# Kernel optimization log

Measured on AMD Instinct MI355X. Metric: run time of the kernel, lower is better.

Reference implementation:

```python
import jax, jax.numpy as jnp
import numpy as np

B, S, HID = 2, 2048, 2048
H, KVH, D = 16, 4, 128
GROUPS = H // KVH
THETA = 10000.0
SCALE = 1.0 / np.sqrt(D).astype(np.float32)
NEG = -1e9


def setup_inputs() -> dict:
    key = jax.random.key(0)
    ks = jax.random.split(key, 6)
    x = jax.random.normal(ks[0], (B, S, HID), dtype=jnp.float32)
    # causal additive mask, broadcast over heads
    causal = jnp.triu(jnp.full((S, S), NEG, dtype=jnp.float32), k=1)
    attn_mask = jnp.broadcast_to(causal, (B, 1, S, S))
    pos_ids = jnp.broadcast_to(jnp.arange(S, dtype=jnp.int32), (B, S))
    sd = 0.02
    Wq = jax.random.normal(ks[1], (H * D, HID), dtype=jnp.float32) * sd
    Wk = jax.random.normal(ks[2], (KVH * D, HID), dtype=jnp.float32) * sd
    Wv = jax.random.normal(ks[3], (KVH * D, HID), dtype=jnp.float32) * sd
    Wo = jax.random.normal(ks[4], (HID, H * D), dtype=jnp.float32) * sd
    return {"x": x, "attn_mask": attn_mask, "pos_ids": pos_ids,
            "Wq": Wq, "Wk": Wk, "Wv": Wv, "Wo": Wo}


def _rope_cos_sin(pos_ids):
    # pos_ids: [B, S] -> cos/sin: [B, 1, S, D]
    inv_freq = 1.0 / (THETA ** (jnp.arange(0, D, 2, dtype=jnp.float32) / D))
    freqs = pos_ids.astype(jnp.float32)[:, :, None] * inv_freq  # [B, S, D/2]
    emb = jnp.concatenate([freqs, freqs], axis=-1)              # [B, S, D]
    return jnp.cos(emb)[:, None], jnp.sin(emb)[:, None]


def _rotate_half(t):
    t1, t2 = jnp.split(t, 2, axis=-1)
    return jnp.concatenate([-t2, t1], axis=-1)


def reference(x, attn_mask, pos_ids, Wq, Wk, Wv, Wo):
    b, s, _ = x.shape
    q = jnp.einsum('bsh,oh->bso', x, Wq).reshape(b, s, H, D).transpose(0, 2, 1, 3)
    k = jnp.einsum('bsh,oh->bso', x, Wk).reshape(b, s, KVH, D).transpose(0, 2, 1, 3)
    v = jnp.einsum('bsh,oh->bso', x, Wv).reshape(b, s, KVH, D).transpose(0, 2, 1, 3)
    cos, sin = _rope_cos_sin(pos_ids)
    q = q * cos + _rotate_half(q) * sin
    k = k * cos + _rotate_half(k) * sin
    # GQA: repeat kv heads
    k = jnp.repeat(k, GROUPS, axis=1)  # [b, H, s, D]
    v = jnp.repeat(v, GROUPS, axis=1)
    scores = jnp.einsum('bhqd,bhkd->bhqk', q, k) * SCALE + attn_mask
    weights = jax.nn.softmax(scores, axis=-1)  # dropout p=0 (eval)
    out = jnp.einsum('bhqk,bhkd->bhqd', weights, v)
    out = out.transpose(0, 2, 1, 3).reshape(b, s, H * D)
    return jnp.einsum('bso,ho->bsh', out, Wo)
```

## Files before the change

### kernel.cpp

```cpp
#include <hip/hip_runtime.h>
#include <hip/hip_bf16.h>
#include <stdint.h>

#define B_   2
#define S_   2048
#define HID_ 2048
#define H_   16
#define KVH_ 4
#define D_   128
#define SCALE_ 0.08838834764831845f
#define QSC_ (SCALE_ * 1.4426950408889634f)

typedef __attribute__((ext_vector_type(8))) short bf16x8;
typedef __attribute__((ext_vector_type(4))) float f32x4;
typedef __attribute__((ext_vector_type(4))) short short4v;

__device__ __forceinline__ void async_copy16(void* lds, const void* g) {
  __builtin_amdgcn_global_load_lds((__attribute__((address_space(1))) void*)(uintptr_t)g,
                                   (__attribute__((address_space(3))) void*)lds, 16, 0, 0);
}

__device__ __forceinline__ short bf16bits(float f) {
  __hip_bfloat16 t = __float2bfloat16(f);
  return __builtin_bit_cast(short, t);
}
__device__ __forceinline__ float bf16tof(short s) {
  return __bfloat162float(__builtin_bit_cast(__hip_bfloat16, s));
}

__global__ __launch_bounds__(256) void f2b_all(const float4* __restrict__ x,
                                               const float4* __restrict__ wq,
                                               const float4* __restrict__ wk,
                                               const float4* __restrict__ wv,
                                               const float4* __restrict__ wo,
                                               short4v* __restrict__ xb,
                                               short4v* __restrict__ wqb,
                                               short4v* __restrict__ wkb,
                                               short4v* __restrict__ wvb,
                                               short4v* __restrict__ wob) {
  int i = blockIdx.x * blockDim.x + threadIdx.x;
  const float4* src; short4v* dst; int off;
  if (i < 2097152)      { src = x;  dst = xb;  off = 0; }
  else if (i < 3145728) { src = wq; dst = wqb; off = 2097152; }
  else if (i < 3407872) { src = wk; dst = wkb; off = 3145728; }
  else if (i < 3670016) { src = wv; dst = wvb; off = 3407872; }
  else                  { src = wo; dst = wob; off = 3670016; }
  int k = i - off;
  float4 v = src[k];
  short4v o;
  o[0] = bf16bits(v.x); o[1] = bf16bits(v.y);
  o[2] = bf16bits(v.z); o[3] = bf16bits(v.w);
  dst[k] = o;
}

template <int MODE>
__global__ __launch_bounds__(256, 2) void gemm_bt(const __hip_bfloat16* __restrict__ A,
                                                  const __hip_bfloat16* __restrict__ Bw,
                                                  void* __restrict__ Cout,
                                                  void* __restrict__ Cout2,
                                                  void* __restrict__ Cout3,
                                                  int M, int N, int K) {
  __shared__ __align__(16) __hip_bfloat16 Asm[2][128 * 64];
  __shared__ __align__(16) __hip_bfloat16 Bsm[2][128 * 64];
  const int tid  = threadIdx.x;
  const int lane = tid & 63;
  const int wid  = tid >> 6;
  const int nwg = gridDim.x * gridDim.y;
  const int id  = blockIdx.y * gridDim.x + blockIdx.x;
  const int swz = (id & 7) * (nwg >> 3) + (id >> 3);
  const int m0 = (swz / gridDim.x) * 128;
  const int n0 = (swz % gridDim.x) * 128;
  const int qm = (wid >> 1) * 64;
  const int qn = (wid & 1) * 64;
  const int ar = lane & 15;
  const int ag = lane >> 4;
  const int srow = tid >> 3;
  const int sun  = tid & 7;

  auto STAGE = [&](int sb, int k0) {
#pragma unroll
    for (int c = 0; c < 4; ++c) {
      const int row = c * 32 + srow;
      const int cu  = sun ^ (row & 7);
      async_copy16(&Asm[sb][c * 2048 + tid * 8], A  + (size_t)(m0 + row) * K + k0 + cu * 8);
      async_copy16(&Bsm[sb][c * 2048 + tid * 8], Bw + (size_t)(n0 + row) * K + k0 + cu * 8);
    }
  };

  f32x4 acc[4][4] = {};

  STAGE(0, 0);
  asm volatile("s_waitcnt vmcnt(0)" ::: "memory");
  __syncthreads();

  int cur = 0;
  for (int k0 = 0; k0 < K; k0 += 64) {
    if (k0 + 64 < K) STAGE(cur ^ 1, k0 + 64);

#pragma unroll
    for (int kk = 0; kk < 2; ++kk) {
      bf16x8 af[4], bfr[4];
#pragma unroll
      for (int i = 0; i < 4; ++i) {
        const int row = qm + i * 16 + ar;
        const int u = (kk * 4 + ag) ^ (row & 7);
        af[i] = *(const bf16x8*)(&Asm[cur][row * 64 + u * 8]);
      }
#pragma unroll
      for (int j = 0; j < 4; ++j) {
        const int row = qn + j * 16 + ar;
        const int u = (kk * 4 + ag) ^ (row & 7);
        bfr[j] = *(const bf16x8*)(&Bsm[cur][row * 64 + u * 8]);
      }
#pragma unroll
      for (int i = 0; i < 4; ++i)
#pragma unroll
        for (int j = 0; j < 4; ++j)
          acc[i][j] = __builtin_amdgcn_mfma_f32_16x16x32_bf16(af[i], bfr[j], acc[i][j], 0, 0, 0);
    }
    asm volatile("s_waitcnt vmcnt(0)" ::: "memory");
    __syncthreads();
    cur ^= 1;
  }

  const int rb = (lane >> 4) * 4;
  const int cl = lane & 15;
#pragma unroll
  for (int i = 0; i < 4; ++i)
#pragma unroll
    for (int j = 0; j < 4; ++j) {
      const int n = n0 + qn + j * 16 + cl;
#pragma unroll
      for (int r = 0; r < 4; ++r) {
        const int m = m0 + qm + i * 16 + rb + r;
        float v = acc[i][j][r];
        if (MODE == 3) {
          ((float*)Cout)[(size_t)m * N + n] = v;
        } else {
          const int bb = m >> 11, ss = m & (S_ - 1);
          if (n < 2048) {
            const int hh = n >> 7, dd = n & 127;
            ((__hip_bfloat16*)Cout)[(((size_t)bb * 16 + hh) * S_ + ss) * D_ + dd] = __float2bfloat16(v);
          } else if (n < 2560) {
            const int n2 = n - 2048, hh = n2 >> 7, dd = n2 & 127;
            ((__hip_bfloat16*)Cout2)[(((size_t)bb * 4 + hh) * S_ + ss) * D_ + dd] = __float2bfloat16(v);
          } else {
            const int n2 = n - 2560, hh = n2 >> 7, dd = n2 & 127;
            ((__hip_bfloat16*)Cout3)[(((size_t)bb * 4 + hh) * D_ + dd) * S_ + ss] = __float2bfloat16(v);
          }
        }
      }
    }
}

__global__ __launch_bounds__(256) void rope_inplace(__hip_bfloat16* __restrict__ buf,
                                                    const int* __restrict__ pos_ids,
                                                    int lognh, float scale) {
  int idx = blockIdx.x * blockDim.x + threadIdx.x;
  int t  = idx & 15;
  int s  = (idx >> 4) & (S_ - 1);
  int bh = idx >> 15;
  int b  = bh >> lognh;
  float pos = (float)pos_ids[b * S_ + s];
  size_t base = ((size_t)bh * S_ + s) * D_ + t * 4;
  short4v lo = *(short4v*)(buf + base);
  short4v hi = *(short4v*)(buf + base + 64);
  short4v lo2, hi2;
#pragma unroll
  for (int e = 0; e < 4; ++e) {
    float d = (float)(t * 4 + e);
    float ang = pos * exp2f(d * -0.20762050593046014f);
    float c = cosf(ang), sn = sinf(ang);
    float lv = bf16tof(lo[e]), hv = bf16tof(hi[e]);
    lo2[e] = bf16bits((lv * c - hv * sn) * scale);
    hi2[e] = bf16bits((hv * c + lv * sn) * scale);
  }
  *(short4v*)(buf + base)      = lo2;
  *(short4v*)(buf + base + 64) = hi2;
}

__global__ __launch_bounds__(256, 2) void flash_attn7(const __hip_bfloat16* __restrict__ Q,
                                                      const __hip_bfloat16* __restrict__ K,
                                                      const __hip_bfloat16* __restrict__ Vt,
                                                      __hip_bfloat16* __restrict__ O) {
  __shared__ __align__(16) __hip_bfloat16 Ksm[2][64 * 128];
  __shared__ __align__(16) __hip_bfloat16 Vsm[2][128 * 64];
  __shared__ __align__(16) __hip_bfloat16 Psm[4][16 * 64];
  const int lane = threadIdx.x & 63;
  const int wid  = threadIdx.x >> 6;
  const int i   = blockIdx.x;
  const int xcd = i & 7;
  const int j   = i >> 3;
  const int bh  = xcd * 4 + (j & 3);
  const int qt  = 31 - (j >> 2);
  const int b   = bh >> 4;
  const int h   = bh & 15;
  const int kvh = h >> 2;
  const int qrow0 = qt * 64 + wid * 16;
  const int ar = lane & 15;
  const int ag = lane >> 4;
  const int q  = qrow0 + ar;
  const int nkv = qt + 1;

  const __hip_bfloat16* Qb = Q  + ((size_t)bh * S_ + qrow0) * D_;
  const __hip_bfloat16* Kb = K  + (size_t)(b * KVH_ + kvh) * S_ * D_;
  const __hip_bfloat16* Vb = Vt + (size_t)(b * KVH_ + kvh) * D_ * S_;

  bf16x8 qf[4];
#pragma unroll
  for (int kf = 0; kf < 4; ++kf)
    qf[kf] = *(const bf16x8*)(Qb + (size_t)ar * D_ + kf * 32 + ag * 8);

  auto STAGE = [&](int sb, int t) {
    const int kv0 = t * 64;
#pragma unroll
    for (int c = 0; c < 4; ++c) {
      const int idx = wid * 4 + c;
      const int rowK = idx * 4 + (lane >> 4);
      const int gcK  = (lane & 15) ^ (rowK & 7);
      async_copy16(&Ksm[sb][idx * 512 + lane * 8],
                   Kb + (size_t)(kv0 + rowK) * D_ + gcK * 8);
      const int rowV = idx * 8 + (lane >> 3);
      const int gcV  = (lane & 7) ^ (rowV & 7);
      async_copy16(&Vsm[sb][idx * 512 + lane * 8],
                   Vb + (size_t)rowV * S_ + kv0 + gcV * 8);
    }
  };

  f32x4 acc[8] = {};
  float l = 0.f;
  char* pb = (char*)&Psm[wid][0];

  STAGE(0, 0);
  asm volatile("s_waitcnt vmcnt(0)" ::: "memory");
  __syncthreads();

  int buf = 0;
  for (int t = 0; t < nkv; ++t, buf ^= 1) {
    if (t + 1 < nkv) STAGE(buf ^ 1, t + 1);
    const int kv0 = t * 64;
    f32x4 st[4] = {};
    const char* kbase = (const char*)&Ksm[buf][0];
    __builtin_amdgcn_s_setprio(1);
#pragma unroll
    for (int kvt = 0; kvt < 4; ++kvt) {
      const int rr = kvt * 16 + ar;
      const int rx = rr & 7;
#pragma unroll
      for (int kf = 0; kf < 4; ++kf) {
        const bf16x8 kfrag = *(const bf16x8*)(kbase + rr * 256 + (((kf * 4 + ag) ^ rx) << 4));
        st[kvt] = __builtin_amdgcn_mfma_f32_16x16x32_bf16(kfrag, qf[kf], st[kvt], 0, 0, 0);
      }
    }
    __builtin_amdgcn_s_setprio(0);
    const bool needmask = (t == nkv - 1);
    float psum = 0.f;
#pragma unroll
    for (int kvt = 0; kvt < 4; ++kvt) {
      short4v pk;
#pragma unroll
      for (int r = 0; r < 4; ++r) {
        float s = st[kvt][r];
        if (needmask && (kv0 + kvt * 16 + ag * 4 + r > q)) s = -3.0e38f;
        const float p = exp2f(s - 8.f);
        psum += p;
        pk[r] = bf16bits(p);
      }
      const int g = kvt * 2 + (ag >> 1);
      *(short4v*)(pb + ar * 128 + ((g ^ (ar & 7)) << 4) + (ag & 1) * 8) = pk;
    }
    psum += __shfl_xor(psum, 16, 64);
    psum += __shfl_xor(psum, 32, 64);
    l += psum;
    asm volatile("s_waitcnt lgkmcnt(0)" ::: "memory");
    const bf16x8 pf0 = *(const bf16x8*)(pb + ar * 128 + ((ag ^ (ar & 7)) << 4));
    const bf16x8 pf1 = *(const bf16x8*)(pb + ar * 128 + (((4 + ag) ^ (ar & 7)) << 4));
    const char* vbase = (const char*)&Vsm[buf][0];
    __builtin_amdgcn_s_setprio(1);
#pragma unroll
    for (int df = 0; df < 8; ++df) {
      const int rr = df * 16 + ar;
      const int rx = rr & 7;
      const bf16x8 v0 = *(const bf16x8*)(vbase + rr * 128 + ((ag ^ rx) << 4));
      const bf16x8 v1 = *(const bf16x8*)(vbase + rr * 128 + (((4 + ag) ^ rx) << 4));
      acc[df] = __builtin_amdgcn_mfma_f32_16x16x32_bf16(v0, pf0, acc[df], 0, 0, 0);
      acc[df] = __builtin_amdgcn_mfma_f32_16x16x32_bf16(v1, pf1, acc[df], 0, 0, 0);
    }
    __builtin_amdgcn_s_setprio(0);
    asm volatile("s_waitcnt vmcnt(0)" ::: "memory");
    __syncthreads();
  }

  const float linv = 1.f / l;
  __hip_bfloat16* Ob = O + ((size_t)b * S_ + qrow0 + ar) * (H_ * D_) + h * D_;
#pragma unroll
  for (int df = 0; df < 8; ++df) {
    short4v o4;
#pragma unroll
    for (int r = 0; r < 4; ++r)
      o4[r] = bf16bits(acc[df][r] * linv);
    *(short4v*)(Ob + df * 16 + ag * 4) = o4;
  }
}

extern "C" void kernel_launch(void* const* d_in, const int* in_sizes, int n_in,
                              void* d_out, int out_size, void* d_ws, size_t ws_size,
                              hipStream_t stream) {
  (void)in_sizes; (void)n_in; (void)out_size; (void)ws_size;
  const float* x  = (const float*)d_in[0];
  const int* pos  = (const int*)d_in[2];
  const float* Wq = (const float*)d_in[3];
  const float* Wk = (const float*)d_in[4];
  const float* Wv = (const float*)d_in[5];
  const float* Wo = (const float*)d_in[6];

  char* ws = (char*)d_ws;
  __hip_bfloat16* xb   = (__hip_bfloat16*)(ws);
  __hip_bfloat16* wqb  = (__hip_bfloat16*)(ws + 16777216);
  __hip_bfloat16* wkb  = (__hip_bfloat16*)(ws + 25165824);
  __hip_bfloat16* wvb  = (__hip_bfloat16*)(ws + 27262976);
  __hip_bfloat16* wob  = (__hip_bfloat16*)(ws + 29360128);
  __hip_bfloat16* qb16 = (__hip_bfloat16*)(ws + 37748736);
  __hip_bfloat16* kb16 = (__hip_bfloat16*)(ws + 54525952);
  __hip_bfloat16* vt16 = (__hip_bfloat16*)(ws + 58720256);
  __hip_bfloat16* attn = (__hip_bfloat16*)(ws + 62914560);

  f2b_all<<<18432, 256, 0, stream>>>((const float4*)x, (const float4*)Wq, (const float4*)Wk,
                                     (const float4*)Wv, (const float4*)Wo,
                                     (short4v*)xb, (short4v*)wqb, (short4v*)wkb,
                                     (short4v*)wvb, (short4v*)wob);

  gemm_bt<5><<<dim3(24, 32), 256, 0, stream>>>(xb, wqb, qb16, kb16, vt16, 4096, 3072, 2048);

  rope_inplace<<<4096, 256, 0, stream>>>(qb16, pos, 4, QSC_);
  rope_inplace<<<1024, 256, 0, stream>>>(kb16, pos, 2, 1.0f);

  flash_attn7<<<1024, 256, 0, stream>>>(qb16, kb16, vt16, attn);

  gemm_bt<3><<<dim3(16, 32), 256, 0, stream>>>(attn, wob, d_out, nullptr, nullptr, 4096, 2048, 2048);
}
```

Measured before the change: 216.6 us.

## Triple-buffer GEMM with K=32 stages and fuse Q/K RoPE launches

The bf16 GEMM moves from double-buffered 64-wide K tiles to triple-buffered 32-wide K tiles. Prefetch now runs two stages ahead, and partial vmcnt waits replace the full drain each iteration. The LDS swizzle is adapted to the 32-column rows, and the occupancy hint of 2 in launch_bounds is dropped. Separately, the two RoPE launches for Q and K are merged into one kernel to save a launch. The GEMM now issues two barriers per 32-wide step, so it synchronises more often per unit of K.

```diff
diff --git a/kernel.cpp b/kernel.cpp
--- a/kernel.cpp
+++ b/kernel.cpp
@@ -54,14 +54,14 @@
 }
 
 template <int MODE>
-__global__ __launch_bounds__(256, 2) void gemm_bt(const __hip_bfloat16* __restrict__ A,
-                                                  const __hip_bfloat16* __restrict__ Bw,
-                                                  void* __restrict__ Cout,
-                                                  void* __restrict__ Cout2,
-                                                  void* __restrict__ Cout3,
-                                                  int M, int N, int K) {
-  __shared__ __align__(16) __hip_bfloat16 Asm[2][128 * 64];
-  __shared__ __align__(16) __hip_bfloat16 Bsm[2][128 * 64];
+__global__ __launch_bounds__(256) void gemm_bt(const __hip_bfloat16* __restrict__ A,
+                                               const __hip_bfloat16* __restrict__ Bw,
+                                               void* __restrict__ Cout,
+                                               void* __restrict__ Cout2,
+                                               void* __restrict__ Cout3,
+                                               int M, int N, int K) {
+  __shared__ __align__(16) __hip_bfloat16 Asm[3][128 * 32];
+  __shared__ __align__(16) __hip_bfloat16 Bsm[3][128 * 32];
   const int tid  = threadIdx.x;
   const int lane = tid & 63;
   const int wid  = tid >> 6;
@@ -74,53 +74,61 @@
   const int qn = (wid & 1) * 64;
   const int ar = lane & 15;
   const int ag = lane >> 4;
-  const int srow = tid >> 3;
-  const int sun  = tid & 7;
 
   auto STAGE = [&](int sb, int k0) {
 #pragma unroll
-    for (int c = 0; c < 4; ++c) {
-      const int row = c * 32 + srow;
-      const int cu  = sun ^ (row & 7);
-      async_copy16(&Asm[sb][c * 2048 + tid * 8], A  + (size_t)(m0 + row) * K + k0 + cu * 8);
-      async_copy16(&Bsm[sb][c * 2048 + tid * 8], Bw + (size_t)(n0 + row) * K + k0 + cu * 8);
+    for (int l = 0; l < 2; ++l) {
+      const int idx = l * 256 + tid;
+      const int row = idx >> 2;
+      const int cu  = (idx & 3) ^ ((row >> 1) & 3);
+      async_copy16(&Asm[sb][idx * 8], A  + (size_t)(m0 + row) * K + k0 + cu * 8);
+      async_copy16(&Bsm[sb][idx * 8], Bw + (size_t)(n0 + row) * K + k0 + cu * 8);
     }
   };
 
   f32x4 acc[4][4] = {};
 
+  auto COMPUTE = [&](int sb) {
+    bf16x8 af[4], bfr[4];
+#pragma unroll
+    for (int i = 0; i < 4; ++i) {
+      const int row = qm + i * 16 + ar;
+      const int u = ag ^ ((row >> 1) & 3);
+      af[i] = *(const bf16x8*)(&Asm[sb][row * 32 + u * 8]);
+    }
+#pragma unroll
+    for (int j = 0; j < 4; ++j) {
+      const int row = qn + j * 16 + ar;
+      const int u = ag ^ ((row >> 1) & 3);
+      bfr[j] = *(const bf16x8*)(&Bsm[sb][row * 32 + u * 8]);
+    }
+#pragma unroll
+    for (int i = 0; i < 4; ++i)
+#pragma unroll
+      for (int j = 0; j < 4; ++j)
+        acc[i][j] = __builtin_amdgcn_mfma_f32_16x16x32_bf16(af[i], bfr[j], acc[i][j], 0, 0, 0);
+  };
+
+  const int T = K >> 5;
   STAGE(0, 0);
-  asm volatile("s_waitcnt vmcnt(0)" ::: "memory");
-  __syncthreads();
+  if (T > 1) STAGE(1, 32);
 
   int cur = 0;
-  for (int k0 = 0; k0 < K; k0 += 64) {
-    if (k0 + 64 < K) STAGE(cur ^ 1, k0 + 64);
-
-#pragma unroll
-    for (int kk = 0; kk < 2; ++kk) {
-      bf16x8 af[4], bfr[4];
-#pragma unroll
-      for (int i = 0; i < 4; ++i) {
-        const int row = qm + i * 16 + ar;
-        const int u = (kk * 4 + ag) ^ (row & 7);
-        af[i] = *(const bf16x8*)(&Asm[cur][row * 64 + u * 8]);
-      }
-#pragma unroll
-      for (int j = 0; j < 4; ++j) {
-        const int row = qn + j * 16 + ar;
-        const int u = (kk * 4 + ag) ^ (row & 7);
-        bfr[j] = *(const bf16x8*)(&Bsm[cur][row * 64 + u * 8]);
-      }
-#pragma unroll
-      for (int i = 0; i < 4; ++i)
-#pragma unroll
-        for (int j = 0; j < 4; ++j)
-          acc[i][j] = __builtin_amdgcn_mfma_f32_16x16x32_bf16(af[i], bfr[j], acc[i][j], 0, 0, 0);
-    }
-    asm volatile("s_waitcnt vmcnt(0)" ::: "memory");
-    __syncthreads();
-    cur ^= 1;
+  for (int t = 0; t < T; ++t) {
+    const int ahead = T - 1 - t;
+    if (ahead >= 2) {
+      int nx = cur + 2; if (nx >= 3) nx -= 3;
+      STAGE(nx, (t + 2) * 32);
+      asm volatile("s_waitcnt vmcnt(8)" ::: "memory");
+    } else if (ahead == 1) {
+      asm volatile("s_waitcnt vmcnt(4)" ::: "memory");
+    } else {
+      asm volatile("s_waitcnt vmcnt(0)" ::: "memory");
+    }
+    __builtin_amdgcn_s_barrier();
+    COMPUTE(cur);
+    __builtin_amdgcn_s_barrier();
+    cur = (cur == 2) ? 0 : cur + 1;
   }
 
   const int rb = (lane >> 4) * 4;
@@ -153,14 +161,21 @@
     }
 }
 
-__global__ __launch_bounds__(256) void rope_inplace(__hip_bfloat16* __restrict__ buf,
-                                                    const int* __restrict__ pos_ids,
-                                                    int lognh, float scale) {
+__global__ __launch_bounds__(256) void rope_all(__hip_bfloat16* __restrict__ qb,
+                                                __hip_bfloat16* __restrict__ kb,
+                                                const int* __restrict__ pos_ids) {
   int idx = blockIdx.x * blockDim.x + threadIdx.x;
-  int t  = idx & 15;
-  int s  = (idx >> 4) & (S_ - 1);
-  int bh = idx >> 15;
-  int b  = bh >> lognh;
+  __hip_bfloat16* buf;
+  float scale;
+  int b, rel;
+  if (idx < 1048576) {
+    rel = idx; buf = qb; scale = QSC_; b = (rel >> 15) >> 4;
+  } else {
+    rel = idx - 1048576; buf = kb; scale = 1.0f; b = (rel >> 15) >> 2;
+  }
+  const int t  = rel & 15;
+  const int s  = (rel >> 4) & (S_ - 1);
+  const int bh = rel >> 15;
   float pos = (float)pos_ids[b * S_ + s];
   size_t base = ((size_t)bh * S_ + s) * D_ + t * 4;
   short4v lo = *(short4v*)(buf + base);
@@ -332,8 +347,7 @@
 
   gemm_bt<5><<<dim3(24, 32), 256, 0, stream>>>(xb, wqb, qb16, kb16, vt16, 4096, 3072, 2048);
 
-  rope_inplace<<<4096, 256, 0, stream>>>(qb16, pos, 4, QSC_);
-  rope_inplace<<<1024, 256, 0, stream>>>(kb16, pos, 2, 1.0f);
+  rope_all<<<5120, 256, 0, stream>>>(qb16, kb16, pos);
 
   flash_attn7<<<1024, 256, 0, stream>>>(qb16, kb16, vt16, attn);
 
```

New measurement: 203.0 us. 6.3% less time.
